# Performance work log

Measured on AMD Instinct MI355X. Metric: run time of the kernel, lower is better.

Reference implementation:

```python
import jax, jax.numpy as jnp
import numpy as np

EPS = 1e-15
MAX_TANH_ARG = 1.0 - 1e-5  # clamp for artanh domain, standard in Poincare-ball libs


def logmap0(x):
    # Poincare ball, c=1: logmap0(x) = artanh(||x||) * x / ||x||
    norm = jnp.linalg.norm(x, axis=-1, keepdims=True)
    norm_c = jnp.clip(norm, EPS, MAX_TANH_ARG)
    scale = jnp.arctanh(norm_c) / jnp.maximum(norm, EPS)
    return scale * x


def expmap0(v):
    # Poincare ball, c=1: expmap0(v) = tanh(||v||) * v / ||v||
    norm = jnp.linalg.norm(v, axis=-1, keepdims=True)
    scale = jnp.tanh(norm) / jnp.maximum(norm, EPS)
    return scale * v


def setup_inputs() -> dict:
    key = jax.random.key(0)
    k1, k2, k3, k4 = jax.random.split(key, 4)
    N, E, D_IN, D_OUT = 50000, 600000, 128, 128
    # points loosely inside/near the ball; logmap0 clamps the norm anyway
    x = jax.random.uniform(k1, (N, D_IN), dtype=jnp.float32)
    edge_index = jax.random.randint(k2, (2, E), 0, N, dtype=jnp.int32)
    W = jax.random.normal(k3, (D_OUT, D_IN), dtype=jnp.float32) / np.sqrt(D_IN)
    b = jax.random.normal(k4, (D_OUT,), dtype=jnp.float32) * 0.01
    return {"x": x, "edge_index": edge_index, "W": W, "b": b}


def reference(x, edge_index, W, b):
    num_nodes = x.shape[0]
    src, dst = edge_index[0], edge_index[1]

    x_tangent = logmap0(x)                       # [N, D_in]
    h = x_tangent @ W.T + b                      # [N, D_out]

    # symmetric degree count: each edge adds 1 to dst and 1 to src
    ones = jnp.ones(src.shape[0], dtype=jnp.float32)
    deg = (jax.ops.segment_sum(ones, dst, num_segments=num_nodes)
           + jax.ops.segment_sum(ones, src, num_segments=num_nodes))
    deg = jnp.maximum(deg, 1.0)
    dinv = deg ** -0.5                           # [N]

    # fused gather-scale-scatter across ALL feature dims at once
    msg = h[src] * (dinv[src] * dinv[dst])[:, None]   # [E, D_out]
    out = jax.ops.segment_sum(msg, dst, num_segments=num_nodes)  # [N, D_out]

    return expmap0(out)
```

## Files before the change

kernel.cpp:

```cpp
#include <hip/hip_runtime.h>
#include <math.h>

#define D 128
#define CAP 48

typedef __attribute__((ext_vector_type(8))) short short8;
typedef __attribute__((ext_vector_type(4))) float f32x4;

__device__ inline unsigned short f2bf(float f) {
  unsigned int u = __float_as_uint(f);
  u = (u + 0x7FFFu + ((u >> 16) & 1u)) >> 16;
  return (unsigned short)u;
}
__device__ inline float bf2f(unsigned int us) {
  return __uint_as_float(us << 16);
}

__global__ __launch_bounds__(256) void k_fused(
    const float* __restrict__ x, const float* __restrict__ W,
    const float* __restrict__ b, const int* __restrict__ src,
    const int* __restrict__ dst, unsigned int* __restrict__ deg,
    int* __restrict__ ebuf, unsigned short* __restrict__ h, int N, int E,
    int ET) {
  __shared__ unsigned short Wl[16 * 128 * 8];
  __shared__ float bs[D];

  const int t = threadIdx.x;
  const int w = t >> 6;
  const int l = t & 63;

  for (int i = t * 4; i < D * D; i += 1024) {
    float4 wv = *(const float4*)(W + i);
    int r = i >> 7, c = i & 127;
    int idx = ((c >> 3) << 10) + (r << 3) + (c & 7);
    *(ushort4*)(&Wl[idx]) =
        make_ushort4(f2bf(wv.x), f2bf(wv.y), f2bf(wv.z), f2bf(wv.w));
  }
  if (t < D) bs[t] = b[t];
  __syncthreads();

  if (w >= 2) {
    for (int e = blockIdx.x * 128 + (t - 128); e < E; e += ET) {
      int d = dst[e], s = src[e];
      unsigned int pos = atomicAdd(&deg[d], 1u) & 0xFFFFu;
      if (pos < CAP) ebuf[(size_t)d * CAP + pos] = s;
      atomicAdd(&deg[s], 0x10000u);
    }
    return;
  }

  const int lc = l & 15;
  const int q = l >> 4;
  const int r0 = blockIdx.x * 32;
  const int grow = r0 + w * 16 + lc;
  const bool ok = grow < N;
  const float* xp = x + (size_t)grow * D + q * 8;

  short8 a[4];
  float ss = 0.0f;
#pragma unroll
  for (int kk = 0; kk < 4; ++kk) {
    float4 u = ok ? *(const float4*)(xp + kk * 32) : make_float4(0, 0, 0, 0);
    float4 v = ok ? *(const float4*)(xp + kk * 32 + 4) : make_float4(0, 0, 0, 0);
    ss += u.x * u.x + u.y * u.y + u.z * u.z + u.w * u.w;
    ss += v.x * v.x + v.y * v.y + v.z * v.z + v.w * v.w;
    short8 af;
    af[0] = (short)f2bf(u.x); af[1] = (short)f2bf(u.y);
    af[2] = (short)f2bf(u.z); af[3] = (short)f2bf(u.w);
    af[4] = (short)f2bf(v.x); af[5] = (short)f2bf(v.y);
    af[6] = (short)f2bf(v.z); af[7] = (short)f2bf(v.w);
    a[kk] = af;
  }
  ss += __shfl_xor(ss, 16, 64);
  ss += __shfl_xor(ss, 32, 64);
  float nrm = sqrtf(ss);
  float nc = fminf(fmaxf(nrm, 1e-15f), 1.0f - 1e-5f);
  float rs = atanhf(nc) / fmaxf(nrm, 1e-15f);

  f32x4 acc[8];
#pragma unroll
  for (int nt = 0; nt < 8; ++nt) acc[nt] = (f32x4){0.f, 0.f, 0.f, 0.f};

#pragma unroll
  for (int kk = 0; kk < 4; ++kk) {
#pragma unroll
    for (int nt = 0; nt < 8; ++nt) {
      short8 bf = *(const short8*)(&Wl[((kk * 4 + q) << 10) + ((nt * 16 + lc) << 3)]);
      acc[nt] = __builtin_amdgcn_mfma_f32_16x16x32_bf16(a[kk], bf, acc[nt], 0, 0, 0);
    }
  }

  float rsl[4];
#pragma unroll
  for (int i = 0; i < 4; ++i) rsl[i] = __shfl(rs, q * 4 + i, 64);

#pragma unroll
  for (int nt = 0; nt < 8; ++nt) {
    int j = nt * 16 + lc;
    float bj = bs[j];
#pragma unroll
    for (int i = 0; i < 4; ++i) {
      int gr = r0 + w * 16 + q * 4 + i;
      if (gr < N) h[(size_t)gr * D + j] = f2bf(rsl[i] * acc[nt][i] + bj);
    }
  }
}

__global__ __launch_bounds__(256) void k_gather(
    const unsigned short* __restrict__ h, const int* __restrict__ ebuf,
    const unsigned int* __restrict__ deg, float* __restrict__ out, int N) {
  int gid = blockIdx.x * 256 + threadIdx.x;
  int r = gid >> 6, l = gid & 63;
  if (r >= N) return;

  unsigned int vr = deg[r];
  int cnt = (int)(vr & 0xFFFFu);
  if (cnt > CAP) cnt = CAP;
  float di_d = rsqrtf(fmaxf((float)((vr & 0xFFFFu) + (vr >> 16)), 1.0f));
  const int* eb = ebuf + (size_t)r * CAP;

  int s_l = (l < cnt) ? eb[l] : 0;
  unsigned int vs = (l < cnt) ? deg[s_l] : 0u;
  float dv_l =
      (l < cnt) ? rsqrtf(fmaxf((float)((vs & 0xFFFFu) + (vs >> 16)), 1.0f)) : 0.0f;

  float ax = 0.0f, ay = 0.0f;
  for (int i = 0; i < cnt; i += 8) {
    unsigned int pv[8];
    float wj[8];
#pragma unroll
    for (int j = 0; j < 8; ++j) {
      int s = __shfl(s_l, i + j, 64);
      wj[j] = __shfl(dv_l, i + j, 64);
      pv[j] = *(const unsigned int*)(h + (size_t)s * D + l * 2);
    }
#pragma unroll
    for (int j = 0; j < 8; ++j) {
      ax += wj[j] * bf2f(pv[j] & 0xFFFFu);
      ay += wj[j] * bf2f(pv[j] >> 16);
    }
  }

  ax *= di_d;
  ay *= di_d;

  float sN = ax * ax + ay * ay;
#pragma unroll
  for (int off = 32; off > 0; off >>= 1) sN += __shfl_down(sN, off, 64);
  sN = __shfl(sN, 0, 64);
  float n = sqrtf(sN);
  float sc = tanhf(n) / fmaxf(n, 1e-15f);

  float2* op = (float2*)(out + (size_t)r * D);
  op[l] = make_float2(ax * sc, ay * sc);
}

extern "C" void kernel_launch(void* const* d_in, const int* in_sizes, int n_in,
                              void* d_out, int out_size, void* d_ws, size_t ws_size,
                              hipStream_t stream) {
  const float* x = (const float*)d_in[0];
  const int* ei = (const int*)d_in[1];
  const float* W = (const float*)d_in[2];
  const float* b = (const float*)d_in[3];
  float* out = (float*)d_out;

  const int N = in_sizes[0] / D;
  const int E = in_sizes[1] / 2;
  const int* src = ei;
  const int* dst = ei + E;

  unsigned short* h = (unsigned short*)d_ws;
  unsigned int* deg = (unsigned int*)(h + (size_t)N * D);
  int* ebuf = (int*)(deg + N);

  hipMemsetAsync(deg, 0, (size_t)N * sizeof(unsigned int), stream);

  const int NB = (N + 31) / 32;
  const int ET = NB * 128;
  k_fused<<<NB, 256, 0, stream>>>(x, W, b, src, dst, deg, ebuf, h, N, E, ET);
  k_gather<<<(int)(((long long)N * 64 + 255) / 256), 256, 0, stream>>>(
      h, ebuf, deg, out, N);
}
```

Measured before the change: 167.9 us.

## Preconvert W to bf16 in a prep kernel, batch edge atomics, widen gather unroll

Adds a prep kernel that zeroes the degree array and converts W to a bf16 MFMA-ready layout once, replacing the memset and the per-block W conversion into shared memory. The fused kernel now reads W fragments and the bias straight from global memory (L2-resident), so it drops the shared-memory fill and the block barrier. The edge-scatter warps issue three edges' loads and atomics together to overlap their latency. The gather loop unrolls 16 neighbours instead of 8 to keep more loads in flight. The cost is an extra kernel launch, global instead of LDS reads for W in the MFMA loop, and higher register pressure in the gather.

```diff
diff --git a/kernel.cpp b/kernel.cpp
--- a/kernel.cpp
+++ b/kernel.cpp
@@ -16,35 +16,58 @@
   return __uint_as_float(us << 16);
 }
 
+__global__ __launch_bounds__(256) void k_prep(const float* __restrict__ W,
+                                              unsigned int* __restrict__ deg,
+                                              unsigned short* __restrict__ Wbf,
+                                              int N) {
+  int t = blockIdx.x * 256 + threadIdx.x;
+  if (t < N) deg[t] = 0u;
+  int i = t * 4;
+  if (i < D * D) {
+    float4 wv = *(const float4*)(W + i);
+    int r = i >> 7, c = i & 127;
+    int idx = ((c >> 3) << 10) + (r << 3) + (c & 7);
+    *(ushort4*)(&Wbf[idx]) =
+        make_ushort4(f2bf(wv.x), f2bf(wv.y), f2bf(wv.z), f2bf(wv.w));
+  }
+}
+
 __global__ __launch_bounds__(256) void k_fused(
-    const float* __restrict__ x, const float* __restrict__ W,
+    const float* __restrict__ x, const unsigned short* __restrict__ Wbf,
     const float* __restrict__ b, const int* __restrict__ src,
     const int* __restrict__ dst, unsigned int* __restrict__ deg,
     int* __restrict__ ebuf, unsigned short* __restrict__ h, int N, int E,
     int ET) {
-  __shared__ unsigned short Wl[16 * 128 * 8];
-  __shared__ float bs[D];
-
   const int t = threadIdx.x;
   const int w = t >> 6;
   const int l = t & 63;
 
-  for (int i = t * 4; i < D * D; i += 1024) {
-    float4 wv = *(const float4*)(W + i);
-    int r = i >> 7, c = i & 127;
-    int idx = ((c >> 3) << 10) + (r << 3) + (c & 7);
-    *(ushort4*)(&Wl[idx]) =
-        make_ushort4(f2bf(wv.x), f2bf(wv.y), f2bf(wv.z), f2bf(wv.w));
-  }
-  if (t < D) bs[t] = b[t];
-  __syncthreads();
-
   if (w >= 2) {
-    for (int e = blockIdx.x * 128 + (t - 128); e < E; e += ET) {
-      int d = dst[e], s = src[e];
-      unsigned int pos = atomicAdd(&deg[d], 1u) & 0xFFFFu;
-      if (pos < CAP) ebuf[(size_t)d * CAP + pos] = s;
-      atomicAdd(&deg[s], 0x10000u);
+    const int base = blockIdx.x * 128 + (t - 128);
+    int dd[3], ssrc[3];
+    bool v[3];
+#pragma unroll
+    for (int i = 0; i < 3; ++i) {
+      int e = base + i * ET;
+      v[i] = (e < E);
+      dd[i] = v[i] ? dst[e] : 0;
+      ssrc[i] = v[i] ? src[e] : 0;
+    }
+    unsigned int pos[3] = {0xFFFFu, 0xFFFFu, 0xFFFFu};
+#pragma unroll
+    for (int i = 0; i < 3; ++i)
+      if (v[i]) pos[i] = atomicAdd(&deg[dd[i]], 1u) & 0xFFFFu;
+#pragma unroll
+    for (int i = 0; i < 3; ++i)
+      if (v[i]) atomicAdd(&deg[ssrc[i]], 0x10000u);
+#pragma unroll
+    for (int i = 0; i < 3; ++i)
+      if (pos[i] < CAP) ebuf[(size_t)dd[i] * CAP + pos[i]] = ssrc[i];
+    for (int e = base + 3 * ET; e < E; e += ET) {
+      int d_ = dst[e], s_ = src[e];
+      unsigned int p = atomicAdd(&deg[d_], 1u) & 0xFFFFu;
+      if (p < CAP) ebuf[(size_t)d_ * CAP + p] = s_;
+      atomicAdd(&deg[s_], 0x10000u);
     }
     return;
   }
@@ -85,7 +108,8 @@
   for (int kk = 0; kk < 4; ++kk) {
 #pragma unroll
     for (int nt = 0; nt < 8; ++nt) {
-      short8 bf = *(const short8*)(&Wl[((kk * 4 + q) << 10) + ((nt * 16 + lc) << 3)]);
+      short8 bf =
+          *(const short8*)(Wbf + ((kk * 4 + q) << 10) + ((nt * 16 + lc) << 3));
       acc[nt] = __builtin_amdgcn_mfma_f32_16x16x32_bf16(a[kk], bf, acc[nt], 0, 0, 0);
     }
   }
@@ -97,7 +121,7 @@
 #pragma unroll
   for (int nt = 0; nt < 8; ++nt) {
     int j = nt * 16 + lc;
-    float bj = bs[j];
+    float bj = b[j];
 #pragma unroll
     for (int i = 0; i < 4; ++i) {
       int gr = r0 + w * 16 + q * 4 + i;
@@ -125,17 +149,17 @@
       (l < cnt) ? rsqrtf(fmaxf((float)((vs & 0xFFFFu) + (vs >> 16)), 1.0f)) : 0.0f;
 
   float ax = 0.0f, ay = 0.0f;
-  for (int i = 0; i < cnt; i += 8) {
-    unsigned int pv[8];
-    float wj[8];
-#pragma unroll
-    for (int j = 0; j < 8; ++j) {
+  for (int i = 0; i < cnt; i += 16) {
+    unsigned int pv[16];
+    float wj[16];
+#pragma unroll
+    for (int j = 0; j < 16; ++j) {
       int s = __shfl(s_l, i + j, 64);
       wj[j] = __shfl(dv_l, i + j, 64);
       pv[j] = *(const unsigned int*)(h + (size_t)s * D + l * 2);
     }
 #pragma unroll
-    for (int j = 0; j < 8; ++j) {
+    for (int j = 0; j < 16; ++j) {
       ax += wj[j] * bf2f(pv[j] & 0xFFFFu);
       ay += wj[j] * bf2f(pv[j] >> 16);
     }
@@ -172,12 +196,17 @@
   unsigned short* h = (unsigned short*)d_ws;
   unsigned int* deg = (unsigned int*)(h + (size_t)N * D);
   int* ebuf = (int*)(deg + N);
-
-  hipMemsetAsync(deg, 0, (size_t)N * sizeof(unsigned int), stream);
+  size_t woff = ((size_t)N * D * 2 + (size_t)N * 4 + (size_t)N * CAP * 4 + 15) &
+                ~(size_t)15;
+  unsigned short* Wbf = (unsigned short*)((char*)d_ws + woff);
+
+  int NPB = (N + 255) / 256;
+  if (NPB < 64) NPB = 64;
+  k_prep<<<NPB, 256, 0, stream>>>(W, deg, Wbf, N);
 
   const int NB = (N + 31) / 32;
   const int ET = NB * 128;
-  k_fused<<<NB, 256, 0, stream>>>(x, W, b, src, dst, deg, ebuf, h, N, E, ET);
+  k_fused<<<NB, 256, 0, stream>>>(x, Wbf, b, src, dst, deg, ebuf, h, N, E, ET);
   k_gather<<<(int)(((long long)N * 64 + 255) / 256), 256, 0, stream>>>(
       h, ebuf, deg, out, N);
 }
```

Measured after the change: 169.9 us. Within noise of the previous version (+1.2%).
